# Kernel tuning notes

Hardware: AMD Instinct MI355X
Metric: run time of the kernel (lower is better)

The kernel has to match this reference:

```python
import jax, jax.numpy as jnp
import numpy as np

Z_DIM = 32
POLY_ORDER = 3
INCLUDE_BIAS = True

# Static index arrays replicating the nested-loop term ordering of the torch code.
_I2, _J2 = np.triu_indices(Z_DIM)  # pairs (i, j) with i <= j, row-major in i -> matches loop order
_TRIPLES = np.array([(i, j, k) for i in range(Z_DIM) for j in range(i, Z_DIM) for k in range(j, Z_DIM)], dtype=np.int32)
_TI, _TJ, _TK = _TRIPLES[:, 0], _TRIPLES[:, 1], _TRIPLES[:, 2]


def build_library(z):
    # z: [B, d] -> Theta: [B, n_terms], same column order as build_library_torch
    B = z.shape[0]
    terms = []
    if INCLUDE_BIAS:
        terms.append(jnp.ones((B, 1), dtype=z.dtype))
    terms.append(z)
    if POLY_ORDER >= 2:
        terms.append(z[:, _I2] * z[:, _J2])  # [B, C(d+1,2)] quadratic terms
    if POLY_ORDER >= 3:
        terms.append(z[:, _TI] * z[:, _TJ] * z[:, _TK])  # [B, C(d+2,3)] cubic terms
    return jnp.concatenate(terms, axis=1)


def setup_inputs() -> dict:
    key = jax.random.key(0)
    k1, k2 = jax.random.split(key)
    B = 65536
    n_terms = 6545  # 1 + 32 + 528 + 5984 for d=32, order=3, bias
    z = jax.random.normal(k1, (B, Z_DIM), dtype=jnp.float32)
    Xi = jax.random.normal(k2, (n_terms, Z_DIM), dtype=jnp.float32)
    Xi_mask = jnp.ones((n_terms, Z_DIM), dtype=jnp.float32)
    z_mean = jnp.zeros((1, Z_DIM), dtype=jnp.float32)
    z_std = jnp.ones((1, Z_DIM), dtype=jnp.float32)
    return {"z": z, "Xi": Xi, "Xi_mask": Xi_mask, "z_mean": z_mean, "z_std": z_std}


def reference(z, Xi, Xi_mask, z_mean, z_std):
    # NOTE: the original module computes z_norm = (z - z_mean) / z_std but
    # never uses it; Theta is built from the raw z. Reproduce exactly.
    Theta = build_library(z)            # [B, n_terms]
    Xi_eff = Xi * Xi_mask               # [n_terms, z_dim]
    dz_dt = Theta @ Xi_eff              # [B, z_dim]
    return dz_dt
```

## Files before the change

### kernel.cpp

```cpp
#include <hip/hip_runtime.h>


#define Z 32
#define ROWS 65536
#define NBLK (ROWS / 128)

#define NCHUNK 552
#define NGRAN (NCHUNK * 2)
#define NGP 1120

typedef float f32x16 __attribute__((ext_vector_type(16)));
typedef _Float16 h2 __attribute__((ext_vector_type(2)));
typedef _Float16 h8 __attribute__((ext_vector_type(8)));

__device__ __forceinline__ h2 pkrtz(float a, float b) {
    return __builtin_bit_cast(h2, __builtin_amdgcn_cvt_pkrtz(a, b));
}

struct Sched {
    unsigned mg[NGP];
    short rt[NGRAN * 8];
    int nq[4];
};

constexpr Sched make_sched() {
    Sched s{};
    short gi[NGP] = {}, gj[NGP] = {};
    char gt[NGP] = {}, gq[NGP] = {};
    int tidx[32][32] = {}, pidx[32] = {};
    {
        int n = 0;
        for (int a = 0; a < 32; ++a)
            for (int b = a; b < 32; ++b) { tidx[a][b] = n; n += 32 - b; }
        for (int i = 0; i < 32; ++i) pidx[i] = i * 32 - i * (i - 1) / 2;
    }
    int g = 0;
    for (int q = 0; q < 4; ++q) {
        int g0 = g;
        for (int b = 0; b < 32; ++b)
            if ((b >> 3) <= q)
                for (int a = 0; a <= b; ++a) { gi[g]=(short)a; gj[g]=(short)b; gt[g]=0; gq[g]=(char)q; ++g; }
        for (int b = 0; b < 32; ++b)
            if ((b >> 3) >= q) { gi[g]=(short)b; gj[g]=32; gt[g]=1; gq[g]=(char)q; ++g; }
        gi[g]=32; gj[g]=32; gt[g]=2; gq[g]=(char)q; ++g;
        while ((g - g0) & 7) { gi[g]=32; gj[g]=32; gt[g]=3; gq[g]=(char)q; ++g; }
        s.nq[q] = (g - g0) / 2;
    }
    for (int gg = 0; gg < NGRAN; ++gg) {
        s.mg[gg] = ((unsigned)gi[gg] * 512u) | (((unsigned)gj[gg] * 512u) << 16);
        int i = gi[gg], j = gj[gg], ty = gt[gg], q = gq[gg];
        for (int jj = 0; jj < 8; ++jj) {
            int k = 8 * q + jj, row = -1;
            if (ty == 0)      { if (k >= j) row = 561 + tidx[i][j] + (k - j); }
            else if (ty == 1) { if (k <= i) row = 33 + pidx[k] + (i - k); }
            else if (ty == 2) { row = 1 + k; }
            s.rt[gg * 8 + jj] = (short)row;
        }
    }
    return s;
}
constexpr Sched S = make_sched();
static_assert(S.nq[0] == 36 && S.nq[1] == 84 && S.nq[2] == 160 && S.nq[3] == 272, "chunk counts");

__global__ void sindy_prep(const float* __restrict__ Xi,
                           const float* __restrict__ Xi_mask,
                           uint2* __restrict__ Bp2, size_t ws_size) {
    __shared__ unsigned short sh[8][32];
    const int tid = threadIdx.x;
    const int jj = tid >> 5, n = tid & 31;
#pragma unroll
    for (int pass = 0; pass < 4; ++pass) {
        int g = blockIdx.x * 4 + pass;
        int row = S.rt[g * 8 + jj];
        float f = 0.0f;
        if (row >= 0) f = Xi[row * Z + n] * Xi_mask[row * Z + n];
        _Float16 hh = (_Float16)f;
        sh[jj][n] = __builtin_bit_cast(unsigned short, hh);
        __syncthreads();
        if (tid < 64) {
            int n2 = tid & 31, rep = tid >> 5;
            unsigned v0 = sh[4*rep+0][n2], v1 = sh[4*rep+1][n2];
            unsigned v2 = sh[4*rep+2][n2], v3 = sh[4*rep+3][n2];
            int c = g >> 1, h = g & 1;
            size_t idx = ((size_t)c * 64 + h * 32 + n2) * 2 + rep;
            if ((idx + 1) * 8 <= ws_size)
                Bp2[idx] = uint2{v0 | (v1 << 16), v2 | (v3 << 16)};
        }
        __syncthreads();
    }
}

__global__ __launch_bounds__(256, 2) void sindy_mfma(const float* __restrict__ z,
                                                     const float* __restrict__ Xi,
                                                     const float* __restrict__ Xi_mask,
                                                     const uint4* __restrict__ Bp,
                                                     float* __restrict__ out) {
    const int lane = threadIdx.x & 63;
    const int kh = threadIdx.x >> 6;
    const int m = lane & 31;
    const int half = lane >> 5;
    const long R = (long)blockIdx.x * 128;

    __shared__ float zs[33][4][32];
    __shared__ float cs[4][32][32];
    __shared__ unsigned mg_sh[NGP];

    for (int t = threadIdx.x; t < NGP; t += 256) mg_sh[t] = S.mg[t];
    for (int idx = threadIdx.x; idx < 1024; idx += 256) {
        int row = idx >> 3, q4 = idx & 7;
        float4 v = ((const float4*)(z + (R + row) * Z))[q4];
        int t = row >> 5, mm = row & 31;
        zs[4*q4+0][t][mm] = v.x; zs[4*q4+1][t][mm] = v.y;
        zs[4*q4+2][t][mm] = v.z; zs[4*q4+3][t][mm] = v.w;
    }
    if (threadIdx.x < 128) zs[32][threadIdx.x >> 5][threadIdx.x & 31] = 1.0f;
    __syncthreads();

    const int c0 = kh * 138;
    const char* zmb = (const char*)&zs[0][0][0] + 4 * m;
    const unsigned* mgh = mg_sh + half;
    const uint4* bpl = Bp + lane;

    auto zprod4 = [&](unsigned ws, float& t0, float& t1, float& t2, float& t3) {
        const char* bi = zmb + (ws & 0xFFFFu);
        const char* bj = zmb + (ws >> 16);
        t0 = *(const float*)(bi +   0) * *(const float*)(bj +   0);
        t1 = *(const float*)(bi + 128) * *(const float*)(bj + 128);
        t2 = *(const float*)(bi + 256) * *(const float*)(bj + 256);
        t3 = *(const float*)(bi + 384) * *(const float*)(bj + 384);
    };

    uint4 b00 = bpl[(size_t)(c0 + 0) * 64], b01 = bpl[(size_t)(c0 + 1) * 64];
    uint4 b10 = bpl[(size_t)(c0 + 2) * 64], b11 = bpl[(size_t)(c0 + 3) * 64];

    const uint4* bptr = bpl + (size_t)(c0 + 4) * 64;
    const unsigned* mgp = mgh + 2 * c0 + 8;

    float pa0, pa1, pa2, pa3, pb0, pb1, pb2, pb3;
    {
        unsigned u0 = mgh[2*c0+0], u1 = mgh[2*c0+2];
        zprod4(u0, pa0, pa1, pa2, pa3);
        zprod4(u1, pb0, pb1, pb2, pb3);
    }
    unsigned w0s = mgh[2*c0+4], w1s = mgh[2*c0+6];

    f32x16 acc0 = {}, acc1 = {}, acc2 = {}, acc3 = {};

    auto seg = [&](int Q, int cbeg, int cfin, bool tail) {
        const char* zq = zmb + Q * 4096;
        h2 zt0_0, zt0_1, zt0_2, zt0_3, zt1_0, zt1_1, zt1_2, zt1_3;
        h2 zt2_0, zt2_1, zt2_2, zt2_3, zt3_0, zt3_1, zt3_2, zt3_3;
        {
#define LDZ(t) \
            { float a0 = *(const float*)(zq + (t)*128 +    0), a1 = *(const float*)(zq + (t)*128 +  512); \
              float a2 = *(const float*)(zq + (t)*128 + 1024), a3 = *(const float*)(zq + (t)*128 + 1536); \
              float a4 = *(const float*)(zq + (t)*128 + 2048), a5 = *(const float*)(zq + (t)*128 + 2560); \
              float a6 = *(const float*)(zq + (t)*128 + 3072), a7 = *(const float*)(zq + (t)*128 + 3584); \
              zt##t##_0 = pkrtz(a0, a1); zt##t##_1 = pkrtz(a2, a3); \
              zt##t##_2 = pkrtz(a4, a5); zt##t##_3 = pkrtz(a6, a7); }
            LDZ(0) LDZ(1) LDZ(2) LDZ(3)
#undef LDZ
        }

#define MKMFMA(t, accv) \
        auto mfma##t = [&](float pp, const uint4& bv) { \
            h2 p2 = pkrtz(pp, pp); \
            union { h2 h[4]; h8 v; } a; \
            a.h[0] = p2 * zt##t##_0; a.h[1] = p2 * zt##t##_1; \
            a.h[2] = p2 * zt##t##_2; a.h[3] = p2 * zt##t##_3; \
            union { uint4 v; h8 h; } b; b.v = bv; \
            accv = __builtin_amdgcn_mfma_f32_32x32x16_f16(a.v, b.h, accv, 0, 0, 0); \
        };
        MKMFMA(0, acc0) MKMFMA(1, acc1) MKMFMA(2, acc2) MKMFMA(3, acc3)
#undef MKMFMA

        const int cend = tail ? cfin - 4 : cfin;
#pragma unroll 2
        for (int c = cbeg; c < cend; c += 2) {
            uint4 n0 = bptr[0], n1 = bptr[64];
            bptr += 128;
            unsigned nw0 = mgp[0], nw1 = mgp[2];
            mgp += 4;
            float qa0, qa1, qa2, qa3, qb0, qb1, qb2, qb3;
            zprod4(w0s, qa0, qa1, qa2, qa3);
            zprod4(w1s, qb0, qb1, qb2, qb3);
            mfma0(pa0, b00); mfma1(pa1, b00); mfma2(pa2, b00); mfma3(pa3, b00);
            mfma0(pb0, b01); mfma1(pb1, b01); mfma2(pb2, b01); mfma3(pb3, b01);
            pa0 = qa0; pa1 = qa1; pa2 = qa2; pa3 = qa3;
            pb0 = qb0; pb1 = qb1; pb2 = qb2; pb3 = qb3;
            w0s = nw0; w1s = nw1;
            b00 = b10; b01 = b11; b10 = n0; b11 = n1;
        }
        if (tail) {
            float qa0, qa1, qa2, qa3, qb0, qb1, qb2, qb3;
            zprod4(w0s, qa0, qa1, qa2, qa3);
            zprod4(w1s, qb0, qb1, qb2, qb3);
            mfma0(pa0, b00); mfma1(pa1, b00); mfma2(pa2, b00); mfma3(pa3, b00);
            mfma0(pb0, b01); mfma1(pb1, b01); mfma2(pb2, b01); mfma3(pb3, b01);
            pa0 = qa0; pa1 = qa1; pa2 = qa2; pa3 = qa3;
            pb0 = qb0; pb1 = qb1; pb2 = qb2; pb3 = qb3;
            b00 = b10; b01 = b11;
            mfma0(pa0, b00); mfma1(pa1, b00); mfma2(pa2, b00); mfma3(pa3, b00);
            mfma0(pb0, b01); mfma1(pb1, b01); mfma2(pb2, b01); mfma3(pb3, b01);
        }
    };

    if (kh == 0)      { seg(0,   0,  36, false); seg(1,  36, 120, false); seg(2, 120, 138, false); }
    else if (kh == 1) { seg(2, 138, 276, false); }
    else if (kh == 2) { seg(2, 276, 280, false); seg(3, 280, 414, false); }
    else              { seg(3, 414, 552, true); }

    if (kh == 3) {
#pragma unroll
        for (int r = 0; r < 16; ++r) {
            int row = (r & 3) + 8 * (r >> 2) + 4 * half;
            cs[0][row][m] = acc0[r]; cs[1][row][m] = acc1[r];
            cs[2][row][m] = acc2[r]; cs[3][row][m] = acc3[r];
        }
    }
    __syncthreads();
    if (kh == 2) {
#pragma unroll
        for (int r = 0; r < 16; ++r) {
            int row = (r & 3) + 8 * (r >> 2) + 4 * half;
            cs[0][row][m] += acc0[r]; cs[1][row][m] += acc1[r];
            cs[2][row][m] += acc2[r]; cs[3][row][m] += acc3[r];
        }
    }
    __syncthreads();
    if (kh == 1) {
#pragma unroll
        for (int r = 0; r < 16; ++r) {
            int row = (r & 3) + 8 * (r >> 2) + 4 * half;
            cs[0][row][m] += acc0[r]; cs[1][row][m] += acc1[r];
            cs[2][row][m] += acc2[r]; cs[3][row][m] += acc3[r];
        }
    }
    __syncthreads();
    if (kh == 0) {
        const float bias = Xi[m] * Xi_mask[m];
#pragma unroll
        for (int r = 0; r < 16; ++r) {
            int row = (r & 3) + 8 * (r >> 2) + 4 * half;
            out[(R +  0 + row) * Z + m] = acc0[r] + cs[0][row][m] + bias;
            out[(R + 32 + row) * Z + m] = acc1[r] + cs[1][row][m] + bias;
            out[(R + 64 + row) * Z + m] = acc2[r] + cs[2][row][m] + bias;
            out[(R + 96 + row) * Z + m] = acc3[r] + cs[3][row][m] + bias;
        }
    }
}

extern "C" void kernel_launch(void* const* d_in, const int* in_sizes, int n_in,
                              void* d_out, int out_size, void* d_ws, size_t ws_size,
                              hipStream_t stream) {
    const float* z       = (const float*)d_in[0];
    const float* Xi      = (const float*)d_in[1];
    const float* Xi_mask = (const float*)d_in[2];
    float* out = (float*)d_out;
    uint4* Bp  = (uint4*)d_ws;

    sindy_prep<<<NGRAN / 4, 256, 0, stream>>>(Xi, Xi_mask, (uint2*)d_ws, ws_size);
    sindy_mfma<<<NBLK, 256, 0, stream>>>(z, Xi, Xi_mask, Bp, out);
}
```

Before: 109.5 us.

## Split K reduction across eight waves per block instead of four

Doubles the block to 512 threads so each of eight waves handles about 69 K-chunks of the library instead of 138, with launch bounds raised to 4 blocks per CU. Partial accumulators are reduced through two shared buffers in parallel pairs, then summed by wave 0. This targets the long serial K loop per wave and should raise latency hiding. In exchange it adds more LDS use, one more barrier stage, and tighter register limits that could force spills.

```diff
diff --git a/kernel.cpp b/kernel.cpp
--- a/kernel.cpp
+++ b/kernel.cpp
@@ -90,7 +90,7 @@
     }
 }
 
-__global__ __launch_bounds__(256, 2) void sindy_mfma(const float* __restrict__ z,
+__global__ __launch_bounds__(512, 4) void sindy_mfma(const float* __restrict__ z,
                                                      const float* __restrict__ Xi,
                                                      const float* __restrict__ Xi_mask,
                                                      const uint4* __restrict__ Bp,
@@ -102,11 +102,12 @@
     const long R = (long)blockIdx.x * 128;
 
     __shared__ float zs[33][4][32];
-    __shared__ float cs[4][32][32];
+    __shared__ float cs_lo[4][32][32];
+    __shared__ float cs_hi[4][32][32];
     __shared__ unsigned mg_sh[NGP];
 
-    for (int t = threadIdx.x; t < NGP; t += 256) mg_sh[t] = S.mg[t];
-    for (int idx = threadIdx.x; idx < 1024; idx += 256) {
+    for (int t = threadIdx.x; t < NGP; t += 512) mg_sh[t] = S.mg[t];
+    for (int idx = threadIdx.x; idx < 1024; idx += 512) {
         int row = idx >> 3, q4 = idx & 7;
         float4 v = ((const float4*)(z + (R + row) * Z))[q4];
         int t = row >> 5, mm = row & 31;
@@ -116,7 +117,8 @@
     if (threadIdx.x < 128) zs[32][threadIdx.x >> 5][threadIdx.x & 31] = 1.0f;
     __syncthreads();
 
-    const int c0 = kh * 138;
+    constexpr int c0_tab[8] = {0, 70, 138, 208, 276, 346, 414, 484};
+    const int c0 = c0_tab[kh];
     const char* zmb = (const char*)&zs[0][0][0] + 4 * m;
     const unsigned* mgh = mg_sh + half;
     const uint4* bpl = Bp + lane;
@@ -205,49 +207,49 @@
         }
     };
 
-    if (kh == 0)      { seg(0,   0,  36, false); seg(1,  36, 120, false); seg(2, 120, 138, false); }
-    else if (kh == 1) { seg(2, 138, 276, false); }
-    else if (kh == 2) { seg(2, 276, 280, false); seg(3, 280, 414, false); }
-    else              { seg(3, 414, 552, true); }
-
-    if (kh == 3) {
-#pragma unroll
-        for (int r = 0; r < 16; ++r) {
-            int row = (r & 3) + 8 * (r >> 2) + 4 * half;
-            cs[0][row][m] = acc0[r]; cs[1][row][m] = acc1[r];
-            cs[2][row][m] = acc2[r]; cs[3][row][m] = acc3[r];
-        }
-    }
-    __syncthreads();
-    if (kh == 2) {
-#pragma unroll
-        for (int r = 0; r < 16; ++r) {
-            int row = (r & 3) + 8 * (r >> 2) + 4 * half;
-            cs[0][row][m] += acc0[r]; cs[1][row][m] += acc1[r];
-            cs[2][row][m] += acc2[r]; cs[3][row][m] += acc3[r];
-        }
-    }
-    __syncthreads();
-    if (kh == 1) {
-#pragma unroll
-        for (int r = 0; r < 16; ++r) {
-            int row = (r & 3) + 8 * (r >> 2) + 4 * half;
-            cs[0][row][m] += acc0[r]; cs[1][row][m] += acc1[r];
-            cs[2][row][m] += acc2[r]; cs[3][row][m] += acc3[r];
-        }
-    }
+    switch (kh) {
+    case 0: seg(0,   0,  36, false); seg(1,  36,  70, false); break;
+    case 1: seg(1,  70, 120, false); seg(2, 120, 138, false); break;
+    case 2: seg(2, 138, 208, false); break;
+    case 3: seg(2, 208, 276, false); break;
+    case 4: seg(2, 276, 280, false); seg(3, 280, 346, false); break;
+    case 5: seg(3, 346, 414, false); break;
+    case 6: seg(3, 414, 484, false); break;
+    default: seg(3, 484, 552, true); break;
+    }
+
+#define CS_W(buf) \
+        for (int r = 0; r < 16; ++r) { \
+            int row = (r & 3) + 8 * (r >> 2) + 4 * half; \
+            buf[0][row][m] = acc0[r]; buf[1][row][m] = acc1[r]; \
+            buf[2][row][m] = acc2[r]; buf[3][row][m] = acc3[r]; }
+#define CS_A(buf) \
+        for (int r = 0; r < 16; ++r) { \
+            int row = (r & 3) + 8 * (r >> 2) + 4 * half; \
+            buf[0][row][m] += acc0[r]; buf[1][row][m] += acc1[r]; \
+            buf[2][row][m] += acc2[r]; buf[3][row][m] += acc3[r]; }
+
+    if (kh == 7) { CS_W(cs_hi) } else if (kh == 3) { CS_W(cs_lo) }
+    __syncthreads();
+    if (kh == 6) { CS_A(cs_hi) } else if (kh == 2) { CS_A(cs_lo) }
+    __syncthreads();
+    if (kh == 5) { CS_A(cs_hi) } else if (kh == 1) { CS_A(cs_lo) }
+    __syncthreads();
+    if (kh == 4) { CS_A(cs_hi) }
     __syncthreads();
     if (kh == 0) {
         const float bias = Xi[m] * Xi_mask[m];
 #pragma unroll
         for (int r = 0; r < 16; ++r) {
             int row = (r & 3) + 8 * (r >> 2) + 4 * half;
-            out[(R +  0 + row) * Z + m] = acc0[r] + cs[0][row][m] + bias;
-            out[(R + 32 + row) * Z + m] = acc1[r] + cs[1][row][m] + bias;
-            out[(R + 64 + row) * Z + m] = acc2[r] + cs[2][row][m] + bias;
-            out[(R + 96 + row) * Z + m] = acc3[r] + cs[3][row][m] + bias;
-        }
-    }
+            out[(R +  0 + row) * Z + m] = acc0[r] + cs_lo[0][row][m] + cs_hi[0][row][m] + bias;
+            out[(R + 32 + row) * Z + m] = acc1[r] + cs_lo[1][row][m] + cs_hi[1][row][m] + bias;
+            out[(R + 64 + row) * Z + m] = acc2[r] + cs_lo[2][row][m] + cs_hi[2][row][m] + bias;
+            out[(R + 96 + row) * Z + m] = acc3[r] + cs_lo[3][row][m] + cs_hi[3][row][m] + bias;
+        }
+    }
+#undef CS_W
+#undef CS_A
 }
 
 extern "C" void kernel_launch(void* const* d_in, const int* in_sizes, int n_in,
@@ -260,5 +262,5 @@
     uint4* Bp  = (uint4*)d_ws;
 
     sindy_prep<<<NGRAN / 4, 256, 0, stream>>>(Xi, Xi_mask, (uint2*)d_ws, ws_size);
-    sindy_mfma<<<NBLK, 256, 0, stream>>>(z, Xi, Xi_mask, Bp, out);
-}
+    sindy_mfma<<<NBLK, 512, 0, stream>>>(z, Xi, Xi_mask, Bp, out);
+}
```

Result: slower. 135.0 us (+23.3%).
